# Kernel optimization log

Hardware: AMD Instinct MI355X
Metric: run time of the kernel (lower is better)

The kernel has to match this reference:

```python
import math
import jax, jax.numpy as jnp
import numpy as np

SIZES = [32.0, 64.0, 128.0]
RATIOS = [0.5, 1.0, 2.0]
SCALES = [1.0, 2.0 ** (1.0 / 3.0), 2.0 ** (2.0 / 3.0)]
A = 27            # anchors per location
K = 100           # num_proposals
MIN_BOX = 1.0
IMG = 256.0       # image_size = (256, 256)


def _base_anchors():
    a = []
    for s in SIZES:
        for r in RATIOS:
            for sc in SCALES:
                w = max(s * sc * math.sqrt(r), MIN_BOX)
                h = max(s * sc / math.sqrt(r), MIN_BOX)
                a.append([-w / 2, -h / 2, w / 2, h / 2])
    return jnp.asarray(np.array(a, dtype=np.float32))  # [A, 4]


def _conv(x, w, b, pad):
    y = jax.lax.conv_general_dilated(
        x, w, window_strides=(1, 1), padding=[(pad, pad), (pad, pad)],
        dimension_numbers=("NCHW", "OIHW", "NCHW"))
    return y + b[None, :, None, None]


def _apply_deltas(deltas, anchors):
    # deltas, anchors: [N, M, 4]
    widths = anchors[..., 2] - anchors[..., 0]
    heights = anchors[..., 3] - anchors[..., 1]
    ctr_x = anchors[..., 0] + 0.5 * widths
    ctr_y = anchors[..., 1] + 0.5 * heights
    dx = deltas[..., 0] / 10.0
    dy = deltas[..., 1] / 10.0
    dw = deltas[..., 2] / 5.0
    dh = deltas[..., 3] / 5.0
    pred_ctr_x = dx * widths + ctr_x
    pred_ctr_y = dy * heights + ctr_y
    pred_w = jnp.maximum(jnp.exp(dw) * widths, MIN_BOX)
    pred_h = jnp.maximum(jnp.exp(dh) * heights, MIN_BOX)
    x1 = jnp.clip(pred_ctr_x - 0.5 * pred_w, 0.0, IMG)
    y1 = jnp.clip(pred_ctr_y - 0.5 * pred_h, 0.0, IMG)
    x2 = jnp.clip(pred_ctr_x + 0.5 * pred_w, 0.0, IMG)
    y2 = jnp.clip(pred_ctr_y + 0.5 * pred_h, 0.0, IMG)
    boxes = jnp.stack([x1, y1, x2, y2], axis=-1)
    invalid = ((x2 - x1) < MIN_BOX) | ((y2 - y1) < MIN_BOX)
    return jnp.where(invalid[..., None], anchors, boxes)


def setup_inputs() -> dict:
    key = jax.random.key(0)
    ks = jax.random.split(key, 6)
    N, C, H, W = 8, 256, 64, 64
    return {
        "p4": jax.random.normal(ks[0], (N, C, H, W), jnp.float32),
        "w1": jax.random.normal(ks[1], (C, C, 3, 3), jnp.float32) * 0.02,
        "b1": jnp.zeros((C,), jnp.float32),
        "w2": jax.random.normal(ks[2], (C, C, 3, 3), jnp.float32) * 0.02,
        "b2": jnp.zeros((C,), jnp.float32),
        "wc": jax.random.normal(ks[3], (A, C, 1, 1), jnp.float32) * 0.02,
        "bc": jnp.zeros((A,), jnp.float32),
        "wb": jax.random.normal(ks[4], (4 * A, C, 1, 1), jnp.float32) * 0.02,
        "bb": jnp.zeros((4 * A,), jnp.float32),
    }


def reference(p4, w1, b1, w2, b2, wc, bc, wb, bb):
    feat = jax.nn.relu(_conv(p4, w1, b1, 1))
    feat = jax.nn.relu(_conv(feat, w2, b2, 1))
    logits = _conv(feat, wc, bc, 0)          # [N, A, H, W]
    bbox_deltas = _conv(feat, wb, bb, 0)     # [N, 4A, H, W]

    N, _, H, W = bbox_deltas.shape
    # [N, A, 4, H, W] -> [N, H, W, A, 4] -> [N, HWA, 4]
    deltas = bbox_deltas.reshape(N, A, 4, H, W).transpose(0, 3, 4, 1, 2).reshape(N, -1, 4)
    obj = logits.transpose(0, 2, 3, 1).reshape(N, -1)   # [N, HWA]

    base = _base_anchors()                               # [A, 4]
    shift_x = (jnp.arange(W, dtype=jnp.float32) + 0.5) * (IMG / W)
    shift_y = (jnp.arange(H, dtype=jnp.float32) + 0.5) * (IMG / H)
    sy, sx = jnp.meshgrid(shift_y, shift_x, indexing="ij")   # [H, W]
    shifts = jnp.stack([sx, sy, sx, sy], axis=-1)            # [H, W, 4]
    all_a = base[None, None, :, :] + shifts[:, :, None, :]   # [H, W, A, 4]
    all_a = jnp.maximum(all_a, 0.0)
    all_a = jnp.concatenate([all_a[..., :2], jnp.minimum(all_a[..., 2:], IMG)], axis=-1)
    anchors = jnp.broadcast_to(all_a.reshape(1, -1, 4), (N, H * W * A, 4))

    boxes = _apply_deltas(deltas, anchors)               # [N, HWA, 4]
    valid = ((boxes[..., 2] > boxes[..., 0] + MIN_BOX) &
             (boxes[..., 3] > boxes[..., 1] + MIN_BOX))
    obj = jnp.where(valid, obj, -jnp.inf)
    _, idx = jax.lax.top_k(obj, K)                       # [N, K]
    sel = jnp.take_along_axis(boxes, idx[..., None], axis=1)   # [N, K, 4]
    sel_valid = ((sel[..., 2] > sel[..., 0] + MIN_BOX) &
                 (sel[..., 3] > sel[..., 1] + MIN_BOX))
    bidx = jnp.broadcast_to(
        jnp.arange(N, dtype=sel.dtype)[:, None, None], (N, K, 1))
    props = jnp.concatenate([bidx, sel], axis=-1)        # [N, K, 5]
    # Original compacts variable-length per image; we pad invalid rows with 0
    props = jnp.where(sel_valid[..., None], props, 0.0)
    return props, feat
```

## Files before the change

### kernel.cpp

```cpp
#include <hip/hip_runtime.h>
#include <hip/hip_bf16.h>
#include <math.h>

#define NN 8
#define CH 256
#define HH 64
#define WW 64
#define AA 27
#define KK 100
#define MM (HH * WW * AA)

typedef __attribute__((ext_vector_type(8))) short short8v;
typedef __attribute__((ext_vector_type(4))) float float4v;

#define SPL 8921088ull
#define WSPL 589824ull

#define ABUF_B 42240
#define BBUF_B 36864
#define LDS_TOTAL (2 * ABUF_B + 2 * BBUF_B)

__global__ void zero_halo(__hip_bfloat16* a3, __hip_bfloat16* f1)
{
    int g = blockIdx.x * 256 + threadIdx.x;
    int arr = g / 66560;
    int rem = g - arr * 66560;
    int n = rem / 8320;
    int rem2 = rem - n * 8320;
    int b = rem2 >> 5;
    int q = rem2 & 31;
    int hp, wp;
    if (b < 66)       { hp = 0;        wp = b; }
    else if (b < 132) { hp = 65;       wp = b - 66; }
    else if (b < 196) { hp = b - 131;  wp = 0; }
    else              { hp = b - 195;  wp = 65; }
    __hip_bfloat16* base = (arr < 3) ? (a3 + (size_t)arr * SPL)
                                     : (f1 + (size_t)(arr - 3) * SPL);
    short8v z = {0, 0, 0, 0, 0, 0, 0, 0};
    *(short8v*)(base + (((size_t)n * 66 + hp) * 66 + wp) * 256 + q * 8) = z;
}

__device__ inline void split3(float x, __hip_bfloat16& h, __hip_bfloat16& m,
                              __hip_bfloat16& l)
{
    h = __float2bfloat16(x);
    float r = x - __bfloat162float(h);
    m = __float2bfloat16(r);
    float r2 = r - __bfloat162float(m);
    l = __float2bfloat16(r2);
}

__global__ __launch_bounds__(256)
void prep_in(const float* __restrict__ in, __hip_bfloat16* __restrict__ a3)
{
    __shared__ float s_t[64][65];
    const int tid = threadIdx.x;
    const int ct = blockIdx.x & 3;
    const int row = (blockIdx.x >> 2) & 63;
    const int n = blockIdx.x >> 8;
    const int ci0 = ct * 64;

    for (int i = tid; i < 64 * 64; i += 256) {
        int ci = i >> 6, px = i & 63;
        s_t[ci][px] = in[((size_t)(n * 256 + ci0 + ci) << 12) + (row << 6) + px];
    }
    __syncthreads();
    for (int i = tid; i < 64 * 64; i += 256) {
        int px = i >> 6, ci = i & 63;
        __hip_bfloat16 h, m, l;
        split3(s_t[ci][px], h, m, l);
        size_t base = (((size_t)n * 66 + row + 1) * 66 + px + 1) * 256 + ci0 + ci;
        a3[base] = h;
        a3[base + SPL] = m;
        a3[base + 2 * SPL] = l;
    }
}

__global__ __launch_bounds__(256)
void prep_w(const float* __restrict__ w, __hip_bfloat16* __restrict__ wT)
{
    int t = blockIdx.x * 256 + threadIdx.x;
    int co = t >> 8, ci = t & 255;
    const float* src = w + (size_t)t * 9;
#pragma unroll
    for (int tap = 0; tap < 9; ++tap) {
        __hip_bfloat16 h, m, l;
        split3(src[tap], h, m, l);
        size_t base = ((size_t)tap * 256 + co) * 256 + ci;
        wT[base] = h;
        wT[base + WSPL] = m;
        wT[base + 2 * WSPL] = l;
    }
}

typedef __attribute__((address_space(3))) unsigned lds_u32;
typedef const __attribute__((address_space(1))) unsigned glb_u32;

#define AB_PTR(I_)  ((__hip_bfloat16*)(smem + (I_) * ABUF_B))
#define BB_PTR(I_)  ((__hip_bfloat16*)(smem + 2 * ABUF_B + (I_) * BBUF_B))

#define STAGE_A(AS_, CI0_, DST_)  do {                                         \
    const __hip_bfloat16* src_ = a3 + (size_t)(AS_) * SPL +                    \
        ((size_t)(n * 66 + rt * 8) * 66) * 256 + (CI0_);                       \
    __hip_bfloat16* dst_ = (DST_);                                             \
    _Pragma("unroll")                                                          \
    for (int it = 0; it < 6; ++it) {                                           \
        int c = it * 512 + tid;                                                \
        if (c < 2640) {                                                        \
            int r_ = c / 264;                                                  \
            int rem_ = c - r_ * 264;                                           \
            int col_ = rem_ >> 2, q_ = rem_ & 3;                               \
            __builtin_amdgcn_global_load_lds(                                  \
                (glb_u32*)(src_ + ((size_t)r_ * 66 + col_) * 256 + q_ * 8),    \
                (lds_u32*)(dst_ + c * 8), 16, 0, 0);                           \
        }                                                                      \
    }                                                                          \
} while (0)

#define STAGE_B(CI0_, DST_)  do {                                             \
    __hip_bfloat16* dst_ = (DST_);                                             \
    _Pragma("unroll")                                                          \
    for (int it = 0; it < 5; ++it) {                                           \
        int c = it * 512 + tid;                                                \
        if (c < 2304) {                                                        \
            int tap_ = c >> 8;                                                 \
            int rem_ = c & 255;                                                \
            int co_ = rem_ >> 2, q_ = rem_ & 3;                                \
            __builtin_amdgcn_global_load_lds(                                  \
                (glb_u32*)(wT + (size_t)tap_ * 65536 +                         \
                           (size_t)(co0 + co_) * 256 + (CI0_) + q_ * 8),       \
                (lds_u32*)(dst_ + c * 8), 16, 0, 0);                           \
        }                                                                      \
    }                                                                          \
} while (0)

#define CONV_COMPUTE(NB_, SB_, BB_)  do {                                      \
    const __hip_bfloat16* sb_ = (SB_);                                         \
    const __hip_bfloat16* bbp_ = (BB_);                                        \
    _Pragma("unroll")                                                          \
    for (int tap = 0; tap < 9; ++tap) {                                        \
        const int dy_ = tap / 3, dx_ = tap % 3;                                \
        short8v af0 = *(const short8v*)(sb_ + ((w + dy_) * 66 +  0 + l15 + dx_) * 32 + l4 * 8); \
        short8v af1 = *(const short8v*)(sb_ + ((w + dy_) * 66 + 16 + l15 + dx_) * 32 + l4 * 8); \
        short8v af2 = *(const short8v*)(sb_ + ((w + dy_) * 66 + 32 + l15 + dx_) * 32 + l4 * 8); \
        short8v af3 = *(const short8v*)(sb_ + ((w + dy_) * 66 + 48 + l15 + dx_) * 32 + l4 * 8); \
                             \
        {                                                                      \
            const __hip_bfloat16* bl_ = bbp_ + tap * 2048 + l15 * 32 + l4 * 8; \
            short8v b0_ = *(const short8v*)(bl_);                              \
            short8v b1_ = *(const short8v*)(bl_ + 512);                        \
            short8v b2_ = *(const short8v*)(bl_ + 1024);                       \
            short8v b3_ = *(const short8v*)(bl_ + 1536);                       \
            acc[0][0] = __builtin_amdgcn_mfma_f32_16x16x32_bf16(af0, b0_, acc[0][0], 0, 0, 0); \
            acc[1][0] = __builtin_amdgcn_mfma_f32_16x16x32_bf16(af1, b0_, acc[1][0], 0, 0, 0); \
            acc[2][0] = __builtin_amdgcn_mfma_f32_16x16x32_bf16(af2, b0_, acc[2][0], 0, 0, 0); \
            acc[3][0] = __builtin_amdgcn_mfma_f32_16x16x32_bf16(af3, b0_, acc[3][0], 0, 0, 0); \
            acc[0][1] = __builtin_amdgcn_mfma_f32_16x16x32_bf16(af0, b1_, acc[0][1], 0, 0, 0); \
            acc[1][1] = __builtin_amdgcn_mfma_f32_16x16x32_bf16(af1, b1_, acc[1][1], 0, 0, 0); \
            acc[2][1] = __builtin_amdgcn_mfma_f32_16x16x32_bf16(af2, b1_, acc[2][1], 0, 0, 0); \
            acc[3][1] = __builtin_amdgcn_mfma_f32_16x16x32_bf16(af3, b1_, acc[3][1], 0, 0, 0); \
            acc[0][2] = __builtin_amdgcn_mfma_f32_16x16x32_bf16(af0, b2_, acc[0][2], 0, 0, 0); \
            acc[1][2] = __builtin_amdgcn_mfma_f32_16x16x32_bf16(af1, b2_, acc[1][2], 0, 0, 0); \
            acc[2][2] = __builtin_amdgcn_mfma_f32_16x16x32_bf16(af2, b2_, acc[2][2], 0, 0, 0); \
            acc[3][2] = __builtin_amdgcn_mfma_f32_16x16x32_bf16(af3, b2_, acc[3][2], 0, 0, 0); \
            acc[0][3] = __builtin_amdgcn_mfma_f32_16x16x32_bf16(af0, b3_, acc[0][3], 0, 0, 0); \
            acc[1][3] = __builtin_amdgcn_mfma_f32_16x16x32_bf16(af1, b3_, acc[1][3], 0, 0, 0); \
            acc[2][3] = __builtin_amdgcn_mfma_f32_16x16x32_bf16(af2, b3_, acc[2][3], 0, 0, 0); \
            acc[3][3] = __builtin_amdgcn_mfma_f32_16x16x32_bf16(af3, b3_, acc[3][3], 0, 0, 0); \
        }                                                                      \
                                   \
        const __hip_bfloat16* wp_ = wbase + (size_t)(tap * 65536 + ci0);       \
        _Pragma("unroll")                                                      \
        for (int bs = 1; bs < (NB_); ++bs) {                                   \
            const __hip_bfloat16* wq_ = wp_ + (size_t)bs * WSPL;               \
            short8v b0_ = *(const short8v*)(wq_);                              \
            short8v b1_ = *(const short8v*)(wq_ + 4096);                       \
            short8v b2_ = *(const short8v*)(wq_ + 8192);                       \
            short8v b3_ = *(const short8v*)(wq_ + 12288);                      \
            acc[0][0] = __builtin_amdgcn_mfma_f32_16x16x32_bf16(af0, b0_, acc[0][0], 0, 0, 0); \
            acc[1][0] = __builtin_amdgcn_mfma_f32_16x16x32_bf16(af1, b0_, acc[1][0], 0, 0, 0); \
            acc[2][0] = __builtin_amdgcn_mfma_f32_16x16x32_bf16(af2, b0_, acc[2][0], 0, 0, 0); \
            acc[3][0] = __builtin_amdgcn_mfma_f32_16x16x32_bf16(af3, b0_, acc[3][0], 0, 0, 0); \
            acc[0][1] = __builtin_amdgcn_mfma_f32_16x16x32_bf16(af0, b1_, acc[0][1], 0, 0, 0); \
            acc[1][1] = __builtin_amdgcn_mfma_f32_16x16x32_bf16(af1, b1_, acc[1][1], 0, 0, 0); \
            acc[2][1] = __builtin_amdgcn_mfma_f32_16x16x32_bf16(af2, b1_, acc[2][1], 0, 0, 0); \
            acc[3][1] = __builtin_amdgcn_mfma_f32_16x16x32_bf16(af3, b1_, acc[3][1], 0, 0, 0); \
            acc[0][2] = __builtin_amdgcn_mfma_f32_16x16x32_bf16(af0, b2_, acc[0][2], 0, 0, 0); \
            acc[1][2] = __builtin_amdgcn_mfma_f32_16x16x32_bf16(af1, b2_, acc[1][2], 0, 0, 0); \
            acc[2][2] = __builtin_amdgcn_mfma_f32_16x16x32_bf16(af2, b2_, acc[2][2], 0, 0, 0); \
            acc[3][2] = __builtin_amdgcn_mfma_f32_16x16x32_bf16(af3, b2_, acc[3][2], 0, 0, 0); \
            acc[0][3] = __builtin_amdgcn_mfma_f32_16x16x32_bf16(af0, b3_, acc[0][3], 0, 0, 0); \
            acc[1][3] = __builtin_amdgcn_mfma_f32_16x16x32_bf16(af1, b3_, acc[1][3], 0, 0, 0); \
            acc[2][3] = __builtin_amdgcn_mfma_f32_16x16x32_bf16(af2, b3_, acc[2][3], 0, 0, 0); \
            acc[3][3] = __builtin_amdgcn_mfma_f32_16x16x32_bf16(af3, b3_, acc[3][3], 0, 0, 0); \
        }                                                                      \
    }                                                                          \
} while (0)

template <int MODE>
__global__ __launch_bounds__(512, 2)
void conv_mfma(const __hip_bfloat16* __restrict__ a3,
               const __hip_bfloat16* __restrict__ wT,
               const float* __restrict__ bias,
               __hip_bfloat16* __restrict__ outb,
               float* __restrict__ outf)
{
    extern __shared__ __align__(16) char smem[];

    const int tid = threadIdx.x;
    const int lane = tid & 63, w = tid >> 6;
    const int l15 = lane & 15, l4 = lane >> 4;
    const int bid = blockIdx.x;
    const int cg = bid & 3, rt = (bid >> 2) & 7, n = bid >> 5;
    const int co0 = cg * 64;
    const int row = rt * 8 + w;

    float4v acc[4][4];
#pragma unroll
    for (int p = 0; p < 4; ++p)
#pragma unroll
        for (int q = 0; q < 4; ++q) acc[p][q] = (float4v){0.f, 0.f, 0.f, 0.f};

    const __hip_bfloat16* wbase = wT + ((size_t)(co0 + l15)) * 256 + l4 * 8;

    STAGE_A(0, 0, AB_PTR(0));
    STAGE_B(0, BB_PTR(0));
    __syncthreads();

    int cur = 0;
    for (int chunk = 0; chunk < 8; ++chunk) {
        const int ci0 = chunk * 32;
        const int bcur = chunk & 1;
        STAGE_A(1, ci0, AB_PTR(cur ^ 1));
        CONV_COMPUTE(3, AB_PTR(cur), BB_PTR(bcur));
        __syncthreads();
        cur ^= 1;
        STAGE_A(2, ci0, AB_PTR(cur ^ 1));
        CONV_COMPUTE(2, AB_PTR(cur), BB_PTR(bcur));
        __syncthreads();
        cur ^= 1;
        if (chunk < 7) {
            STAGE_A(0, ci0 + 32, AB_PTR(cur ^ 1));
            STAGE_B(ci0 + 32, BB_PTR(bcur ^ 1));
        }
        CONV_COMPUTE(1, AB_PTR(cur), BB_PTR(bcur));
        __syncthreads();
        cur ^= 1;
    }

    float bco[4];
#pragma unroll
    for (int q = 0; q < 4; ++q) bco[q] = bias[co0 + q * 16 + l15];

    if (MODE == 0) {
#pragma unroll
        for (int p = 0; p < 4; ++p)
#pragma unroll
            for (int q = 0; q < 4; ++q) {
#pragma unroll
                for (int v = 0; v < 4; ++v) {
                    float y = fmaxf(acc[p][q][v] + bco[q], 0.f);
                    __hip_bfloat16 h, m, l;
                    split3(y, h, m, l);
                    size_t base = (((size_t)n * 66 + row + 1) * 66 +
                                   p * 16 + l4 * 4 + v + 1) * 256 + co0 + q * 16 + l15;
                    outb[base] = h;
                    outb[base + SPL] = m;
                    outb[base + 2 * SPL] = l;
                }
            }
    } else {
#pragma unroll
        for (int p = 0; p < 4; ++p)
#pragma unroll
            for (int q = 0; q < 4; ++q) {
                float4v y;
#pragma unroll
                for (int v = 0; v < 4; ++v) y[v] = fmaxf(acc[p][q][v] + bco[q], 0.f);
                *(float4v*)(outf + ((size_t)(n * 256 + co0 + q * 16 + l15) << 12) +
                            row * 64 + p * 16 + l4 * 4) = y;
            }
    }
}

__global__ __launch_bounds__(256, 2)
void conv1x1_kernel(const float* __restrict__ feat, const float* __restrict__ wc,
                    const float* __restrict__ bc, const float* __restrict__ wb,
                    const float* __restrict__ bb, float* __restrict__ tmp)
{
    __shared__ float s_f[64][64];
    __shared__ float s_w[64][137];

    const int tid  = threadIdx.x;
    const int n    = blockIdx.x >> 6;
    const int px0  = (blockIdx.x & 63) << 6;
    const int lane = tid & 63;
    const int g    = tid >> 6;

    float acc[34];
#pragma unroll
    for (int k = 0; k < 34; ++k) acc[k] = 0.f;

    for (int chb = 0; chb < 4; ++chb) {
        const int ci0 = chb << 6;
        __syncthreads();
        for (int i = tid; i < 64 * 64; i += 256) {
            int ci = i >> 6, pp = i & 63;
            s_f[ci][pp] = feat[(((size_t)n * CH + ci0 + ci) << 12) + px0 + pp];
        }
        for (int i = tid; i < 135 * 64; i += 256) {
            int co = i >> 6, ci = i & 63;
            float wv = (co < 27) ? wc[(size_t)co * CH + ci0 + ci]
                                 : wb[(size_t)(co - 27) * CH + ci0 + ci];
            s_w[ci][co] = wv;
        }
        __syncthreads();
        for (int ci = 0; ci < 64; ++ci) {
            float f = s_f[ci][lane];
#pragma unroll
            for (int k = 0; k < 34; ++k) {
                int co = g * 34 + k;
                acc[k] += f * s_w[ci][co < 135 ? co : 134];
            }
        }
    }
#pragma unroll
    for (int k = 0; k < 34; ++k) {
        int co = g * 34 + k;
        if (co < 135) {
            float b = (co < 27) ? bc[co] : bb[co - 27];
            tmp[((size_t)n * 135 + co) * 4096 + px0 + lane] = acc[k] + b;
        }
    }
}

__global__ void boxes_kernel(const float* __restrict__ tmp,
                             float* __restrict__ scores, float* __restrict__ boxes)
{
    const int n = blockIdx.y;
    const int i = blockIdx.x * 256 + threadIdx.x;
    const int a = i >> 12;
    const int p = i & 4095;

    const float* t = tmp + (size_t)n * 135 * 4096;
    float logit = t[(size_t)a * 4096 + p];
    float d0 = t[((size_t)(27 + a * 4 + 0)) * 4096 + p];
    float d1 = t[((size_t)(27 + a * 4 + 1)) * 4096 + p];
    float d2 = t[((size_t)(27 + a * 4 + 2)) * 4096 + p];
    float d3 = t[((size_t)(27 + a * 4 + 3)) * 4096 + p];

    const int hh = p >> 6, ww = p & 63;
    const int si = a / 9, ri = (a / 3) % 3, sci = a % 3;

    double s  = (si == 0) ? 32.0 : (si == 1 ? 64.0 : 128.0);
    double r  = (ri == 0) ? 0.5 : (ri == 1 ? 1.0 : 2.0);
    double sv = (sci == 0) ? 1.0 : (sci == 1 ? pow(2.0, 1.0 / 3.0) : pow(2.0, 2.0 / 3.0));
    double sq = sqrt(r);
    float wa = (float)fmax(s * sv * sq, 1.0);
    float ha = (float)fmax(s * sv / sq, 1.0);
    float bx1 = -0.5f * wa, by1 = -0.5f * ha, bx2 = 0.5f * wa, by2 = 0.5f * ha;

    float sx = ((float)ww + 0.5f) * 4.0f;
    float sy = ((float)hh + 0.5f) * 4.0f;
    float ax1 = fmaxf(bx1 + sx, 0.f);
    float ay1 = fmaxf(by1 + sy, 0.f);
    float ax2 = fminf(fmaxf(bx2 + sx, 0.f), 256.f);
    float ay2 = fminf(fmaxf(by2 + sy, 0.f), 256.f);

    float wdt = ax2 - ax1, hgt = ay2 - ay1;
    float cx = ax1 + 0.5f * wdt, cy = ay1 + 0.5f * hgt;
    float dx = d0 / 10.f, dy = d1 / 10.f, dw = d2 / 5.f, dh = d3 / 5.f;
    float pcx = dx * wdt + cx, pcy = dy * hgt + cy;
    float pw = fmaxf(expf(dw) * wdt, 1.f);
    float ph = fmaxf(expf(dh) * hgt, 1.f);
    float x1 = fminf(fmaxf(pcx - 0.5f * pw, 0.f), 256.f);
    float y1 = fminf(fmaxf(pcy - 0.5f * ph, 0.f), 256.f);
    float x2 = fminf(fmaxf(pcx + 0.5f * pw, 0.f), 256.f);
    float y2 = fminf(fmaxf(pcy + 0.5f * ph, 0.f), 256.f);

    bool inval = ((x2 - x1) < 1.f) || ((y2 - y1) < 1.f);
    float fx1 = inval ? ax1 : x1, fy1 = inval ? ay1 : y1;
    float fx2 = inval ? ax2 : x2, fy2 = inval ? ay2 : y2;
    bool valid = (fx2 > fx1 + 1.f) && (fy2 > fy1 + 1.f);

    const int m = p * 27 + a;
    scores[(size_t)n * MM + m] = valid ? logit : -INFINITY;
    float4 bx = make_float4(fx1, fy1, fx2, fy2);
    *(float4*)&boxes[((size_t)n * MM + m) * 4] = bx;
}

__device__ inline unsigned ordf(float f)
{
    unsigned u = __float_as_uint(f);
    return (u & 0x80000000u) ? ~u : (u | 0x80000000u);
}

__global__ void topk_props(const float* __restrict__ scores,
                           const float* __restrict__ boxes,
                           float* __restrict__ props)
{
    const int n = blockIdx.x;
    const int tid = threadIdx.x;
    const float* sc = scores + (size_t)n * MM;

    __shared__ unsigned hist[256];
    __shared__ unsigned u_prefix, u_need, cnt;
    __shared__ unsigned long long selk[100];
    __shared__ unsigned wave_tot[16];

    if (tid == 0) { u_prefix = 0; u_need = 100; cnt = 0; }
    __syncthreads();

    for (int pass = 0; pass < 4; ++pass) {
        if (tid < 256) hist[tid] = 0;
        __syncthreads();
        unsigned pf = u_prefix;
        int shift = 24 - pass * 8;
        for (int i = tid; i < MM; i += 1024) {
            unsigned o = ordf(sc[i]);
            bool match = (pass == 0) || ((o >> (shift + 8)) == (pf >> (shift + 8)));
            if (match) atomicAdd(&hist[(o >> shift) & 255u], 1u);
        }
        __syncthreads();
        if (tid == 0) {
            unsigned nd = u_need;
            int b = 255;
            for (;;) {
                unsigned cb = hist[b];
                if (nd <= cb || b == 0) break;
                nd -= cb;
                --b;
            }
            u_need = nd;
            u_prefix = pf | ((unsigned)b << shift);
        }
        __syncthreads();
    }
    const unsigned T = u_prefix;
    const int need = (int)u_need;
    const int cgt = 100 - need;

    for (int i = tid; i < MM; i += 1024) {
        unsigned o = ordf(sc[i]);
        if (o > T) {
            unsigned pz = atomicAdd(&cnt, 1u);
            selk[pz] = ((unsigned long long)o << 32) | (unsigned long long)(~(unsigned)i);
        }
    }
    __syncthreads();

    unsigned hv = 0;
    for (int base = 0; base < MM; base += 1024) {
        int i = base + tid;
        unsigned o = ordf(sc[i]);
        bool f = (o == T);
        unsigned long long bal = __ballot(f);
        if ((tid & 63) == 0) wave_tot[tid >> 6] = (unsigned)__popcll(bal);
        __syncthreads();
        unsigned wbase = 0, tot = 0;
        int wv = tid >> 6;
        for (int w2 = 0; w2 < 16; ++w2) {
            unsigned cw = wave_tot[w2];
            tot += cw;
            if (w2 < wv) wbase += cw;
        }
        if (f) {
            unsigned rk = hv + wbase +
                          (unsigned)__popcll(bal & ((1ull << (tid & 63)) - 1ull));
            if (rk < (unsigned)need)
                selk[cgt + rk] =
                    ((unsigned long long)o << 32) | (unsigned long long)(~(unsigned)i);
        }
        hv += tot;
        __syncthreads();
        if (hv >= (unsigned)need) break;
    }
    __syncthreads();

    if (tid < 100) {
        unsigned long long k = selk[tid];
        int rank = 0;
        for (int j = 0; j < 100; ++j) rank += (selk[j] > k) ? 1 : 0;
        unsigned idx = ~(unsigned)(k & 0xFFFFFFFFull);
        const float* bx = boxes + ((size_t)n * MM + idx) * 4;
        float x1 = bx[0], y1 = bx[1], x2 = bx[2], y2 = bx[3];
        bool v = (x2 > x1 + 1.f) && (y2 > y1 + 1.f);
        float* o = props + ((size_t)n * 100 + rank) * 5;
        o[0] = v ? (float)n : 0.f;
        o[1] = v ? x1 : 0.f;
        o[2] = v ? y1 : 0.f;
        o[3] = v ? x2 : 0.f;
        o[4] = v ? y2 : 0.f;
    }
}

extern "C" void kernel_launch(void* const* d_in, const int* in_sizes, int n_in,
                              void* d_out, int out_size, void* d_ws, size_t ws_size,
                              hipStream_t stream)
{
    const float* p4 = (const float*)d_in[0];
    const float* w1 = (const float*)d_in[1];
    const float* b1 = (const float*)d_in[2];
    const float* w2 = (const float*)d_in[3];
    const float* b2 = (const float*)d_in[4];
    const float* wc = (const float*)d_in[5];
    const float* bc = (const float*)d_in[6];
    const float* wb = (const float*)d_in[7];
    const float* bb = (const float*)d_in[8];

    float* out   = (float*)d_out;
    float* props = out;
    float* feat  = out + 4000;

    char* ws = (char*)d_ws;
    __hip_bfloat16* a3p = (__hip_bfloat16*)ws;
    __hip_bfloat16* f1p = (__hip_bfloat16*)(ws + 53526528);
    __hip_bfloat16* wt1 = (__hip_bfloat16*)(ws + 107053056);
    __hip_bfloat16* wt2 = (__hip_bfloat16*)(ws + 110592000);
    float* tmp    = (float*)ws;
    float* scores = (float*)(ws + 17694720);
    float* boxesb = (float*)(ws + 21233664);

    zero_halo<<<1560, 256, 0, stream>>>(a3p, f1p);
    prep_w<<<256, 256, 0, stream>>>(w1, wt1);
    prep_w<<<256, 256, 0, stream>>>(w2, wt2);
    prep_in<<<2048, 256, 0, stream>>>(p4, a3p);
    conv_mfma<0><<<256, 512, LDS_TOTAL, stream>>>(a3p, wt1, b1, f1p, nullptr);
    conv_mfma<1><<<256, 512, LDS_TOTAL, stream>>>(f1p, wt2, b2, nullptr, feat);
    conv1x1_kernel<<<512, 256, 0, stream>>>(feat, wc, bc, wb, bb, tmp);
    dim3 g2(432, 8);
    boxes_kernel<<<g2, 256, 0, stream>>>(tmp, scores, boxesb);
    topk_props<<<8, 1024, 0, stream>>>(scores, boxesb, props);
}
```

Measured before the change: 930.8 us.

## Retile conv blocks to 4 rows x 128 output channels with single-buffered weights

Each conv block now covers 4 output rows and 128 output channels instead of 8 rows and 64 channels. The 8 waves split into two halves over channel groups, so each staged activation tile is reused across twice as many output channels. The weight tile grows to 72KB and is single-buffered, reloaded behind an extra barrier after compute instead of overlapping with it. LDS use rises to about 124KB, so occupancy drops to one block per CU.

```diff
diff --git a/kernel.cpp b/kernel.cpp
--- a/kernel.cpp
+++ b/kernel.cpp
@@ -16,9 +16,9 @@
 #define SPL 8921088ull
 #define WSPL 589824ull
 
-#define ABUF_B 42240
-#define BBUF_B 36864
-#define LDS_TOTAL (2 * ABUF_B + 2 * BBUF_B)
+#define ABUF_B 25344
+#define BBUF_B 73728
+#define LDS_TOTAL (2 * ABUF_B + BBUF_B)
 
 __global__ void zero_halo(__hip_bfloat16* a3, __hip_bfloat16* f1)
 {
@@ -97,16 +97,16 @@
 typedef const __attribute__((address_space(1))) unsigned glb_u32;
 
 #define AB_PTR(I_)  ((__hip_bfloat16*)(smem + (I_) * ABUF_B))
-#define BB_PTR(I_)  ((__hip_bfloat16*)(smem + 2 * ABUF_B + (I_) * BBUF_B))
+#define BB_PTR     ((__hip_bfloat16*)(smem + 2 * ABUF_B))
 
 #define STAGE_A(AS_, CI0_, DST_)  do {                                         \
     const __hip_bfloat16* src_ = a3 + (size_t)(AS_) * SPL +                    \
-        ((size_t)(n * 66 + rt * 8) * 66) * 256 + (CI0_);                       \
+        ((size_t)(n * 66 + rt * 4) * 66) * 256 + (CI0_);                       \
     __hip_bfloat16* dst_ = (DST_);                                             \
     _Pragma("unroll")                                                          \
-    for (int it = 0; it < 6; ++it) {                                           \
+    for (int it = 0; it < 4; ++it) {                                           \
         int c = it * 512 + tid;                                                \
-        if (c < 2640) {                                                        \
+        if (c < 1584) {                                                        \
             int r_ = c / 264;                                                  \
             int rem_ = c - r_ * 264;                                           \
             int col_ = rem_ >> 2, q_ = rem_ & 3;                               \
@@ -117,14 +117,14 @@
     }                                                                          \
 } while (0)
 
-#define STAGE_B(CI0_, DST_)  do {                                             \
-    __hip_bfloat16* dst_ = (DST_);                                             \
+#define STAGE_B(CI0_)  do {                                                    \
+    __hip_bfloat16* dst_ = BB_PTR;                                             \
     _Pragma("unroll")                                                          \
-    for (int it = 0; it < 5; ++it) {                                           \
+    for (int it = 0; it < 9; ++it) {                                           \
         int c = it * 512 + tid;                                                \
-        if (c < 2304) {                                                        \
-            int tap_ = c >> 8;                                                 \
-            int rem_ = c & 255;                                                \
+        {                                                                      \
+            int tap_ = c >> 9;                                                 \
+            int rem_ = c & 511;                                                \
             int co_ = rem_ >> 2, q_ = rem_ & 3;                                \
             __builtin_amdgcn_global_load_lds(                                  \
                 (glb_u32*)(wT + (size_t)tap_ * 65536 +                         \
@@ -134,19 +134,20 @@
     }                                                                          \
 } while (0)
 
-#define CONV_COMPUTE(NB_, SB_, BB_)  do {                                      \
+#define CONV_COMPUTE(NB_, SB_)  do {                                           \
     const __hip_bfloat16* sb_ = (SB_);                                         \
-    const __hip_bfloat16* bbp_ = (BB_);                                        \
+    const __hip_bfloat16* bbp_ = BB_PTR;                                       \
     _Pragma("unroll")                                                          \
     for (int tap = 0; tap < 9; ++tap) {                                        \
         const int dy_ = tap / 3, dx_ = tap % 3;                                \
-        short8v af0 = *(const short8v*)(sb_ + ((w + dy_) * 66 +  0 + l15 + dx_) * 32 + l4 * 8); \
-        short8v af1 = *(const short8v*)(sb_ + ((w + dy_) * 66 + 16 + l15 + dx_) * 32 + l4 * 8); \
-        short8v af2 = *(const short8v*)(sb_ + ((w + dy_) * 66 + 32 + l15 + dx_) * 32 + l4 * 8); \
-        short8v af3 = *(const short8v*)(sb_ + ((w + dy_) * 66 + 48 + l15 + dx_) * 32 + l4 * 8); \
+        short8v af0 = *(const short8v*)(sb_ + (((w & 3) + dy_) * 66 +  0 + l15 + dx_) * 32 + l4 * 8); \
+        short8v af1 = *(const short8v*)(sb_ + (((w & 3) + dy_) * 66 + 16 + l15 + dx_) * 32 + l4 * 8); \
+        short8v af2 = *(const short8v*)(sb_ + (((w & 3) + dy_) * 66 + 32 + l15 + dx_) * 32 + l4 * 8); \
+        short8v af3 = *(const short8v*)(sb_ + (((w & 3) + dy_) * 66 + 48 + l15 + dx_) * 32 + l4 * 8); \
                              \
         {                                                                      \
-            const __hip_bfloat16* bl_ = bbp_ + tap * 2048 + l15 * 32 + l4 * 8; \
+            const __hip_bfloat16* bl_ = bbp_ + tap * 4096 +                    \
+                (cohalf * 64 + l15) * 32 + l4 * 8;                             \
             short8v b0_ = *(const short8v*)(bl_);                              \
             short8v b1_ = *(const short8v*)(bl_ + 512);                        \
             short8v b2_ = *(const short8v*)(bl_ + 1024);                       \
@@ -198,7 +199,7 @@
 } while (0)
 
 template <int MODE>
-__global__ __launch_bounds__(512, 2)
+__global__ __launch_bounds__(512, 1)
 void conv_mfma(const __hip_bfloat16* __restrict__ a3,
                const __hip_bfloat16* __restrict__ wT,
                const float* __restrict__ bias,
@@ -210,10 +211,11 @@
     const int tid = threadIdx.x;
     const int lane = tid & 63, w = tid >> 6;
     const int l15 = lane & 15, l4 = lane >> 4;
+    const int cohalf = w >> 2;
     const int bid = blockIdx.x;
-    const int cg = bid & 3, rt = (bid >> 2) & 7, n = bid >> 5;
-    const int co0 = cg * 64;
-    const int row = rt * 8 + w;
+    const int cg = bid & 1, rt = (bid >> 1) & 15, n = bid >> 5;
+    const int co0 = cg * 128;
+    const int row = rt * 4 + (w & 3);
 
     float4v acc[4][4];
 #pragma unroll
@@ -221,36 +223,36 @@
 #pragma unroll
         for (int q = 0; q < 4; ++q) acc[p][q] = (float4v){0.f, 0.f, 0.f, 0.f};
 
-    const __hip_bfloat16* wbase = wT + ((size_t)(co0 + l15)) * 256 + l4 * 8;
+    const __hip_bfloat16* wbase = wT + ((size_t)(co0 + cohalf * 64 + l15)) * 256 + l4 * 8;
 
     STAGE_A(0, 0, AB_PTR(0));
-    STAGE_B(0, BB_PTR(0));
+    STAGE_B(0);
     __syncthreads();
 
     int cur = 0;
     for (int chunk = 0; chunk < 8; ++chunk) {
         const int ci0 = chunk * 32;
-        const int bcur = chunk & 1;
         STAGE_A(1, ci0, AB_PTR(cur ^ 1));
-        CONV_COMPUTE(3, AB_PTR(cur), BB_PTR(bcur));
+        CONV_COMPUTE(3, AB_PTR(cur));
         __syncthreads();
         cur ^= 1;
         STAGE_A(2, ci0, AB_PTR(cur ^ 1));
-        CONV_COMPUTE(2, AB_PTR(cur), BB_PTR(bcur));
+        CONV_COMPUTE(2, AB_PTR(cur));
         __syncthreads();
         cur ^= 1;
+        if (chunk < 7) STAGE_A(0, ci0 + 32, AB_PTR(cur ^ 1));
+        CONV_COMPUTE(1, AB_PTR(cur));
+        __syncthreads();
         if (chunk < 7) {
-            STAGE_A(0, ci0 + 32, AB_PTR(cur ^ 1));
-            STAGE_B(ci0 + 32, BB_PTR(bcur ^ 1));
-        }
-        CONV_COMPUTE(1, AB_PTR(cur), BB_PTR(bcur));
-        __syncthreads();
+            STAGE_B(ci0 + 32);
+            __syncthreads();
+        }
         cur ^= 1;
     }
 
     float bco[4];
 #pragma unroll
-    for (int q = 0; q < 4; ++q) bco[q] = bias[co0 + q * 16 + l15];
+    for (int q = 0; q < 4; ++q) bco[q] = bias[co0 + cohalf * 64 + q * 16 + l15];
 
     if (MODE == 0) {
 #pragma unroll
@@ -263,7 +265,8 @@
                     __hip_bfloat16 h, m, l;
                     split3(y, h, m, l);
                     size_t base = (((size_t)n * 66 + row + 1) * 66 +
-                                   p * 16 + l4 * 4 + v + 1) * 256 + co0 + q * 16 + l15;
+                                   p * 16 + l4 * 4 + v + 1) * 256 +
+                                  co0 + cohalf * 64 + q * 16 + l15;
                     outb[base] = h;
                     outb[base + SPL] = m;
                     outb[base + 2 * SPL] = l;
@@ -277,7 +280,7 @@
                 float4v y;
 #pragma unroll
                 for (int v = 0; v < 4; ++v) y[v] = fmaxf(acc[p][q][v] + bco[q], 0.f);
-                *(float4v*)(outf + ((size_t)(n * 256 + co0 + q * 16 + l15) << 12) +
+                *(float4v*)(outf + ((size_t)(n * 256 + co0 + cohalf * 64 + q * 16 + l15) << 12) +
                             row * 64 + p * 16 + l4 * 4) = y;
             }
     }
```

Measured after the change: 910.4 us. 1.02x faster.
